# Performance work log

Hardware: AMD Instinct MI355X
Metric: run time of the kernel (lower is better)

Reference implementation:

```python
import jax, jax.numpy as jnp
import numpy as np

INPUT, HIDDEN, LAYERS, OUT = 512, 512, 2, 512
B, T = 128, 1024


def _gru_cell(x, h, w_ih, w_hh, b_ih, b_hh):
    # x: [B, D_in], h: [B, H]; w_ih: [3H, D_in], w_hh: [3H, H]
    gi = x @ w_ih.T + b_ih
    gh = h @ w_hh.T + b_hh
    i_r, i_z, i_n = jnp.split(gi, 3, axis=-1)
    h_r, h_z, h_n = jnp.split(gh, 3, axis=-1)
    r = jax.nn.sigmoid(i_r + h_r)
    z = jax.nn.sigmoid(i_z + h_z)
    n = jnp.tanh(i_n + r * h_n)
    return (1.0 - z) * n + z * h


def setup_inputs() -> dict:
    key = jax.random.key(0)
    ks = jax.random.split(key, 11)
    s = 1.0 / np.sqrt(HIDDEN)
    u = lambda k, shp: jax.random.uniform(k, shp, jnp.float32, -s, s)
    return {
        "x": jax.random.normal(ks[0], (B, T, INPUT), jnp.float32),
        "w_ih0": u(ks[1], (3 * HIDDEN, INPUT)),
        "w_hh0": u(ks[2], (3 * HIDDEN, HIDDEN)),
        "b_ih0": u(ks[3], (3 * HIDDEN,)),
        "b_hh0": u(ks[4], (3 * HIDDEN,)),
        "w_ih1": u(ks[5], (3 * HIDDEN, HIDDEN)),
        "w_hh1": u(ks[6], (3 * HIDDEN, HIDDEN)),
        "b_ih1": u(ks[7], (3 * HIDDEN,)),
        "b_hh1": u(ks[8], (3 * HIDDEN,)),
        "fc_w": u(ks[9], (OUT, HIDDEN)),
        "fc_b": u(ks[10], (OUT,)),
    }


def reference(x, w_ih0, w_hh0, b_ih0, b_hh0, w_ih1, w_hh1, b_ih1, b_hh1, fc_w, fc_b):
    xs = jnp.swapaxes(x, 0, 1)  # [T, B, INPUT]
    h0 = jnp.zeros((x.shape[0], HIDDEN), x.dtype)
    h1 = jnp.zeros((x.shape[0], HIDDEN), x.dtype)

    def step(carry, x_t):
        h0, h1 = carry
        h0 = _gru_cell(x_t, h0, w_ih0, w_hh0, b_ih0, b_hh0)
        h1 = _gru_cell(h0, h1, w_ih1, w_hh1, b_ih1, b_hh1)
        return (h0, h1), None

    (h0, h1), _ = jax.lax.scan(step, (h0, h1), xs)
    # final hidden of top layer -> fc (matches outs[-1].squeeze(); B>1 so squeeze is no-op)
    return h1 @ fc_w.T + fc_b
```

## Files before the change

### kernel.cpp

```cpp
#include <hip/hip_runtime.h>


#define TS   1024
#define HID  512
#define NWG  256
#define WGT  256

typedef __attribute__((ext_vector_type(8))) short bf16x8;
typedef __attribute__((ext_vector_type(4))) unsigned short u16x4;
typedef __attribute__((ext_vector_type(4))) float f32x4;

#define WS_SEQ      0
#define WS_FIN      2048
#define WS_HBUF     8192
#define HBUF_ELEMS  65536
#define WS_H1F      (WS_HBUF + 8 * HBUF_ELEMS * 2)
#define WS_ZERO     (WS_HBUF + 8 * HBUF_ELEMS * 2)

__device__ __forceinline__ unsigned short f2bf(float f) {
    unsigned u = __float_as_uint(f);
    u += 0x7FFFu + ((u >> 16) & 1u);
    return (unsigned short)(u >> 16);
}
__device__ __forceinline__ float bf2f(unsigned short s) {
    return __uint_as_float(((unsigned)s) << 16);
}
__device__ __forceinline__ float sigm(float v) { return 1.0f / (1.0f + __expf(-v)); }
__device__ __forceinline__ float tanh_(float v) { return 1.0f - 2.0f / (1.0f + __expf(2.0f * v)); }

__device__ __forceinline__ void st_llc8(void* p, unsigned long long v) {
    asm volatile("global_store_dwordx2 %0, %1, off sc0 sc1" :: "v"(p), "v"(v) : "memory");
}
__device__ __forceinline__ void st_llc16(void* p, f32x4 v) {
    asm volatile("global_store_dwordx4 %0, %1, off sc0 sc1" :: "v"(p), "v"(v) : "memory");
}
__device__ __forceinline__ bf16x8 ld_coh16(const unsigned short* p) {
    const unsigned long long* q = (const unsigned long long*)p;
    union { unsigned long long u[2]; bf16x8 v; } r;
    r.u[0] = __hip_atomic_load(q,     __ATOMIC_RELAXED, __HIP_MEMORY_SCOPE_AGENT);
    r.u[1] = __hip_atomic_load(q + 1, __ATOMIC_RELAXED, __HIP_MEMORY_SCOPE_AGENT);
    return r.v;
}
__device__ __forceinline__ f32x4 ld_coh16f(const float* p) {
    const unsigned long long* q = (const unsigned long long*)p;
    union { unsigned long long u[2]; f32x4 v; } r;
    r.u[0] = __hip_atomic_load(q,     __ATOMIC_RELAXED, __HIP_MEMORY_SCOPE_AGENT);
    r.u[1] = __hip_atomic_load(q + 1, __ATOMIC_RELAXED, __HIP_MEMORY_SCOPE_AGENT);
    return r.v;
}

__global__ void __launch_bounds__(WGT, 1)
gru_persistent(const float* __restrict__ x,
               const float* __restrict__ wi0, const float* __restrict__ wh0,
               const float* __restrict__ bi0, const float* __restrict__ bh0,
               const float* __restrict__ wi1, const float* __restrict__ wh1,
               const float* __restrict__ bi1, const float* __restrict__ bh1,
               const float* __restrict__ fcw, const float* __restrict__ fcb,
               float* __restrict__ out, unsigned char* __restrict__ ws)
{
    __shared__ float ldsRed[3][64][52];

    const int tid   = threadIdx.x;
    const int lane  = tid & 63;
    const int kq    = tid >> 6;
    const int wgid  = blockIdx.x;
    const int layer = wgid >> 7;
    const int wid   = wgid & 127;
    const int mt    = wid & 3;
    const int nt    = wid >> 2;
    const int l15   = lane & 15;
    const int l4    = lane >> 4;
    const int tile0 = mt * 2;
    const int gidx  = layer * 32 + nt;

    unsigned* seqA = (unsigned*)(ws + WS_SEQ + (size_t)mt * 256);
    unsigned* fin  = (unsigned*)(ws + WS_FIN);
    unsigned short* hbm = (unsigned short*)(ws + WS_HBUF);
    float* h1f = (float*)(ws + WS_H1F);

    unsigned short* h0hi[2] = { hbm + 0 * HBUF_ELEMS, hbm + 1 * HBUF_ELEMS };
    unsigned short* h0lo[2] = { hbm + 2 * HBUF_ELEMS, hbm + 3 * HBUF_ELEMS };
    unsigned short* h1hi[2] = { hbm + 4 * HBUF_ELEMS, hbm + 5 * HBUF_ELEMS };
    unsigned short* h1lo[2] = { hbm + 6 * HBUF_ELEMS, hbm + 7 * HBUF_ELEMS };

    bf16x8 wiR[4][3], whR[4][3];
    {
        const float* Wi = layer ? wi1 : wi0;
        const float* Wh = layer ? wh1 : wh0;
        #pragma unroll
        for (int kk = 0; kk < 4; ++kk) {
            const int kc = (kq << 2) + kk;
            #pragma unroll
            for (int g = 0; g < 3; ++g) {
                const int jg = g * HID + nt * 16 + l15;
                const float* pi = Wi + (size_t)jg * HID + kc * 32 + (l4 << 3);
                const float* ph = Wh + (size_t)jg * HID + kc * 32 + (l4 << 3);
                #pragma unroll
                for (int e = 0; e < 8; ++e) {
                    wiR[kk][g][e] = (short)f2bf(pi[e]);
                    whR[kk][g][e] = (short)f2bf(ph[e]);
                }
            }
        }
    }

    float br[4] = {0,0,0,0}, bz[4] = {0,0,0,0}, bni[4] = {0,0,0,0}, bnh[4] = {0,0,0,0};
    if (kq == 0) {
        const float* Bi = layer ? bi1 : bi0;
        const float* Bh = layer ? bh1 : bh0;
        int c0 = nt * 16 + (l4 << 2);
        #pragma unroll
        for (int r = 0; r < 4; ++r) {
            int j = c0 + r;
            br[r]  = Bi[j] + Bh[j];
            bz[r]  = Bi[HID + j] + Bh[HID + j];
            bni[r] = Bi[2 * HID + j];
            bnh[r] = Bh[2 * HID + j];
        }
    }

    float hold[2][4] = {{0,0,0,0},{0,0,0,0}};
    f32x4 acc_i[2][3], acc_h[2][3];
    #pragma unroll
    for (int m2 = 0; m2 < 2; ++m2)
        #pragma unroll
        for (int g = 0; g < 3; ++g) {
            acc_i[m2][g] = (f32x4){0.f,0.f,0.f,0.f};
            acc_h[m2][g] = (f32x4){0.f,0.f,0.f,0.f};
        }

    auto splitPack = [](float a, float b, unsigned& hiw, unsigned& low) {
        unsigned ba = __float_as_uint(a), bb = __float_as_uint(b);
        unsigned ha = ba & 0xFFFF0000u,   hb = bb & 0xFFFF0000u;
        float la = a - __uint_as_float(ha);
        float lb = b - __uint_as_float(hb);
        hiw = (ba >> 16) | hb;
        low = (__float_as_uint(la) >> 16) | (__float_as_uint(lb) & 0xFFFF0000u);
    };

    auto l0_input_mfma = [&](int sn) {
        #pragma unroll
        for (int kk = 0; kk < 4; ++kk) {
            const int kc = (kq << 2) + kk;
            #pragma unroll
            for (int m2 = 0; m2 < 2; ++m2) {
                const int m = (tile0 + m2) * 16 + l15;
                const int k = kc * 32 + (l4 << 3);
                const float* xp = x + ((size_t)m * TS + sn) * HID + k;
                f32x4 xa = *(const f32x4*)xp;
                f32x4 xb = *(const f32x4*)(xp + 4);
                union { unsigned u[4]; bf16x8 v; } hi, lo;
                splitPack(xa[0], xa[1], hi.u[0], lo.u[0]);
                splitPack(xa[2], xa[3], hi.u[1], lo.u[1]);
                splitPack(xb[0], xb[1], hi.u[2], lo.u[2]);
                splitPack(xb[2], xb[3], hi.u[3], lo.u[3]);
                #pragma unroll
                for (int g = 0; g < 3; ++g) {
                    acc_i[m2][g] = __builtin_amdgcn_mfma_f32_16x16x32_bf16(wiR[kk][g], lo.v, acc_i[m2][g], 0, 0, 0);
                    acc_i[m2][g] = __builtin_amdgcn_mfma_f32_16x16x32_bf16(wiR[kk][g], hi.v, acc_i[m2][g], 0, 0, 0);
                }
            }
        }
    };

    __syncthreads();
    if (layer == 0) l0_input_mfma(0);

    for (int s = 0; s <= TS; ++s) {
        const int wp = s & 1, rp = wp ^ 1;
        const bool active = layer ? (s >= 1) : (s < TS);
        if (active) {
            #pragma unroll
            for (int m2 = 0; m2 < 2; ++m2)
                #pragma unroll
                for (int g = 0; g < 3; ++g) {
                    acc_h[m2][g] = (f32x4){0.f,0.f,0.f,0.f};
                    if (layer) acc_i[m2][g] = (f32x4){0.f,0.f,0.f,0.f};
                }

            const unsigned short* pIhi = h0hi[rp];
            const unsigned short* pIlo = h0lo[rp];
            const unsigned short* pHhi = layer ? h1hi[rp] : h0hi[rp];
            const unsigned short* pHlo = layer ? h1lo[rp] : h0lo[rp];

            #pragma unroll
            for (int kk = 0; kk < 4; ++kk) {
                const int kc = (kq << 2) + kk;
                #pragma unroll
                for (int m2 = 0; m2 < 2; ++m2) {
                    const int fo = ((((tile0 + m2) * 16 + kc) * 64) + lane) * 8;
                    bf16x8 vHhi = ld_coh16(pHhi + fo);
                    bf16x8 vHlo = ld_coh16(pHlo + fo);
                    if (layer) {
                        bf16x8 vIhi = ld_coh16(pIhi + fo);
                        bf16x8 vIlo = ld_coh16(pIlo + fo);
                        #pragma unroll
                        for (int g = 0; g < 3; ++g) {
                            acc_i[m2][g] = __builtin_amdgcn_mfma_f32_16x16x32_bf16(wiR[kk][g], vIlo, acc_i[m2][g], 0, 0, 0);
                            acc_i[m2][g] = __builtin_amdgcn_mfma_f32_16x16x32_bf16(wiR[kk][g], vIhi, acc_i[m2][g], 0, 0, 0);
                        }
                    }
                    #pragma unroll
                    for (int g = 0; g < 3; ++g) {
                        acc_h[m2][g] = __builtin_amdgcn_mfma_f32_16x16x32_bf16(whR[kk][g], vHlo, acc_h[m2][g], 0, 0, 0);
                        acc_h[m2][g] = __builtin_amdgcn_mfma_f32_16x16x32_bf16(whR[kk][g], vHhi, acc_h[m2][g], 0, 0, 0);
                    }
                }
            }

            if (kq != 0) {
                float* p = &ldsRed[kq - 1][lane][0];
                #pragma unroll
                for (int m2 = 0; m2 < 2; ++m2)
                    #pragma unroll
                    for (int g = 0; g < 3; ++g) {
                        *(f32x4*)(p + m2 * 24 + g * 4)      = acc_i[m2][g];
                        *(f32x4*)(p + m2 * 24 + 12 + g * 4) = acc_h[m2][g];
                    }
            }
            __syncthreads();
            if (kq == 0) {
                #pragma unroll
                for (int q = 0; q < 3; ++q) {
                    const float* p = &ldsRed[q][lane][0];
                    #pragma unroll
                    for (int m2 = 0; m2 < 2; ++m2)
                        #pragma unroll
                        for (int g = 0; g < 3; ++g) {
                            acc_i[m2][g] += *(const f32x4*)(p + m2 * 24 + g * 4);
                            acc_h[m2][g] += *(const f32x4*)(p + m2 * 24 + 12 + g * 4);
                        }
                }
                unsigned short* dsthi = layer ? h1hi[wp] : h0hi[wp];
                unsigned short* dstlo = layer ? h1lo[wp] : h0lo[wp];
                const int klocal0 = ((nt & 1) << 4) + (l4 << 2);
                const int lanep = l15 | ((klocal0 >> 3) << 4);
                const int chunk = nt >> 1;
                #pragma unroll
                for (int m2 = 0; m2 < 2; ++m2) {
                    u16x4 shi, slo; f32x4 hv;
                    #pragma unroll
                    for (int r = 0; r < 4; ++r) {
                        float vr = acc_i[m2][0][r] + acc_h[m2][0][r] + br[r];
                        float vz = acc_i[m2][1][r] + acc_h[m2][1][r] + bz[r];
                        float rg = sigm(vr);
                        float zg = sigm(vz);
                        float ng = tanh_(acc_i[m2][2][r] + bni[r] + rg * (acc_h[m2][2][r] + bnh[r]));
                        float h  = (1.0f - zg) * ng + zg * hold[m2][r];
                        hold[m2][r] = h;
                        hv[r] = h;
                        unsigned short hb = f2bf(h);
                        shi[r] = hb;
                        slo[r] = f2bf(h - bf2f(hb));
                    }
                    const int eo = ((((tile0 + m2) * 16 + chunk) * 64) + lanep) * 8 + (klocal0 & 7);
                    st_llc8(dsthi + eo, __builtin_bit_cast(unsigned long long, shi));
                    st_llc8(dstlo + eo, __builtin_bit_cast(unsigned long long, slo));
                    if (layer && s == TS) {
                        const int m = (tile0 + m2) * 16 + l15;
                        const int kg0 = nt * 16 + (l4 << 2);
                        st_llc16(h1f + (size_t)m * HID + kg0, hv);
                    }
                }
            }
        }

        if (tid == 0) {
            asm volatile("s_waitcnt vmcnt(0)" ::: "memory");
            __hip_atomic_store(&seqA[gidx], (unsigned)(s + 1),
                               __ATOMIC_RELAXED, __HIP_MEMORY_SCOPE_AGENT);
        }

        if (layer == 0 && s + 1 < TS) {
            #pragma unroll
            for (int m2 = 0; m2 < 2; ++m2)
                #pragma unroll
                for (int g = 0; g < 3; ++g)
                    acc_i[m2][g] = (f32x4){0.f,0.f,0.f,0.f};
            l0_input_mfma(s + 1);
        }

        if (kq == 0) {
            const unsigned long long* sp =
                (const unsigned long long*)(seqA + ((lane & 15) << 2));
            const unsigned tgt = (unsigned)(s + 1);
            for (;;) {
                unsigned long long a = __hip_atomic_load(sp,     __ATOMIC_RELAXED, __HIP_MEMORY_SCOPE_AGENT);
                unsigned long long b = __hip_atomic_load(sp + 1, __ATOMIC_RELAXED, __HIP_MEMORY_SCOPE_AGENT);
                bool ok = ((unsigned)a >= tgt) && ((unsigned)(a >> 32) >= tgt) &&
                          ((unsigned)b >= tgt) && ((unsigned)(b >> 32) >= tgt);
                if (__all(ok)) break;
                __builtin_amdgcn_s_sleep(1);
            }
        }
        __syncthreads();
    }

    if (tid == 0) {
        asm volatile("s_waitcnt vmcnt(0)" ::: "memory");
        __hip_atomic_fetch_add(fin, 1u, __ATOMIC_RELAXED, __HIP_MEMORY_SCOPE_AGENT);
    }
    if (wgid < 64) {
        float* fw = (float*)ldsRed;
        const float* src = fcw + (size_t)wgid * 8 * HID;
        for (int i = tid; i < (8 * HID) / 4; i += WGT) {
            f32x4 v = *(const f32x4*)(src + i * 4);
            int row = (i * 4) >> 9;
            int kk  = (i * 4) & 511;
            *(f32x4*)(fw + row * 516 + kk) = v;
        }
        if (tid == 0) {
            while (__hip_atomic_load(fin, __ATOMIC_RELAXED, __HIP_MEMORY_SCOPE_AGENT) < (unsigned)NWG)
                __builtin_amdgcn_s_sleep(1);
        }
        __syncthreads();
        const int col = wgid * 8 + (tid & 7);
        const int m0  = tid >> 3;
        float a0 = fcb[col], a1 = a0, a2 = a0, a3 = a0;
        const float* fwr = fw + (tid & 7) * 516;
        for (int k = 0; k < HID; k += 4) {
            f32x4 wv  = *(const f32x4*)(fwr + k);
            f32x4 h0v = ld_coh16f(h1f + (size_t)(m0)      * HID + k);
            f32x4 h1v = ld_coh16f(h1f + (size_t)(m0 + 32) * HID + k);
            f32x4 h2v = ld_coh16f(h1f + (size_t)(m0 + 64) * HID + k);
            f32x4 h3v = ld_coh16f(h1f + (size_t)(m0 + 96) * HID + k);
            a0 += h0v[0]*wv[0] + h0v[1]*wv[1] + h0v[2]*wv[2] + h0v[3]*wv[3];
            a1 += h1v[0]*wv[0] + h1v[1]*wv[1] + h1v[2]*wv[2] + h1v[3]*wv[3];
            a2 += h2v[0]*wv[0] + h2v[1]*wv[1] + h2v[2]*wv[2] + h2v[3]*wv[3];
            a3 += h3v[0]*wv[0] + h3v[1]*wv[1] + h3v[2]*wv[2] + h3v[3]*wv[3];
        }
        out[(size_t)(m0)      * HID + col] = a0;
        out[(size_t)(m0 + 32) * HID + col] = a1;
        out[(size_t)(m0 + 64) * HID + col] = a2;
        out[(size_t)(m0 + 96) * HID + col] = a3;
    }
}

extern "C" void kernel_launch(void* const* d_in, const int* in_sizes, int n_in,
                              void* d_out, int out_size, void* d_ws, size_t ws_size,
                              hipStream_t stream) {
    (void)in_sizes; (void)n_in; (void)out_size; (void)ws_size;
    hipMemsetAsync(d_ws, 0, WS_ZERO, stream);
    gru_persistent<<<dim3(NWG), dim3(WGT), 0, stream>>>(
        (const float*)d_in[0],
        (const float*)d_in[1], (const float*)d_in[2],
        (const float*)d_in[3], (const float*)d_in[4],
        (const float*)d_in[5], (const float*)d_in[6],
        (const float*)d_in[7], (const float*)d_in[8],
        (const float*)d_in[9], (const float*)d_in[10],
        (float*)d_out, (unsigned char*)d_ws);
}
```

Before: 8.967 ms.

## Retile GRU work-groups to one M-tile by two N-tiles with batched coherent loads

Each work-group now owns one 16-row batch tile and 32 hidden columns per layer instead of two batch tiles by 16 columns. That doubles the register-resident weight fragments, halves the h-state loads per step, and shrinks each sync group to 16 producers per M-tile. The h-state and next-step x loads are now issued together as wide dwordx4 inline-asm loads followed by a single vmcnt wait, so their latency overlaps, replacing the serialized atomic 8-byte loads. The cost is higher VGPR pressure from the 6-fragment weight arrays, plus a flag poll that now reads only 8 lanes.

```diff
diff --git a/kernel.cpp b/kernel.cpp
--- a/kernel.cpp
+++ b/kernel.cpp
@@ -10,7 +10,6 @@
 typedef __attribute__((ext_vector_type(4))) unsigned short u16x4;
 typedef __attribute__((ext_vector_type(4))) float f32x4;
 
-#define WS_SEQ      0
 #define WS_FIN      2048
 #define WS_HBUF     8192
 #define HBUF_ELEMS  65536
@@ -34,12 +33,15 @@
 __device__ __forceinline__ void st_llc16(void* p, f32x4 v) {
     asm volatile("global_store_dwordx4 %0, %1, off sc0 sc1" :: "v"(p), "v"(v) : "memory");
 }
-__device__ __forceinline__ bf16x8 ld_coh16(const unsigned short* p) {
-    const unsigned long long* q = (const unsigned long long*)p;
-    union { unsigned long long u[2]; bf16x8 v; } r;
-    r.u[0] = __hip_atomic_load(q,     __ATOMIC_RELAXED, __HIP_MEMORY_SCOPE_AGENT);
-    r.u[1] = __hip_atomic_load(q + 1, __ATOMIC_RELAXED, __HIP_MEMORY_SCOPE_AGENT);
-    return r.v;
+__device__ __forceinline__ void ld_coh16_issue(bf16x8& d, const unsigned short* p) {
+    asm volatile("global_load_dwordx4 %0, %1, off sc0 sc1" : "=v"(d) : "v"(p));
+}
+__device__ __forceinline__ void ld16_issue(f32x4& d, const float* p) {
+    asm volatile("global_load_dwordx4 %0, %1, off" : "=v"(d) : "v"(p));
+}
+__device__ __forceinline__ void wait_vm0() {
+    asm volatile("s_waitcnt vmcnt(0)" ::: "memory");
+    __builtin_amdgcn_sched_barrier(0);
 }
 __device__ __forceinline__ f32x4 ld_coh16f(const float* p) {
     const unsigned long long* q = (const unsigned long long*)p;
@@ -58,7 +60,7 @@
                const float* __restrict__ fcw, const float* __restrict__ fcb,
                float* __restrict__ out, unsigned char* __restrict__ ws)
 {
-    __shared__ float ldsRed[3][64][52];
+    __shared__ float ldsRed[3][64][49];
 
     const int tid   = threadIdx.x;
     const int lane  = tid & 63;
@@ -66,14 +68,13 @@
     const int wgid  = blockIdx.x;
     const int layer = wgid >> 7;
     const int wid   = wgid & 127;
-    const int mt    = wid & 3;
-    const int nt    = wid >> 2;
+    const int mtile = wid & 7;
+    const int ntile = wid >> 3;
     const int l15   = lane & 15;
     const int l4    = lane >> 4;
-    const int tile0 = mt * 2;
-    const int gidx  = layer * 32 + nt;
-
-    unsigned* seqA = (unsigned*)(ws + WS_SEQ + (size_t)mt * 256);
+    const int gidx  = layer * 16 + ntile;
+
+    unsigned* seqA = (unsigned*)(ws + (size_t)mtile * 256);
     unsigned* fin  = (unsigned*)(ws + WS_FIN);
     unsigned short* hbm = (unsigned short*)(ws + WS_HBUF);
     float* h1f = (float*)(ws + WS_H1F);
@@ -83,7 +84,7 @@
     unsigned short* h1hi[2] = { hbm + 4 * HBUF_ELEMS, hbm + 5 * HBUF_ELEMS };
     unsigned short* h1lo[2] = { hbm + 6 * HBUF_ELEMS, hbm + 7 * HBUF_ELEMS };
 
-    bf16x8 wiR[4][3], whR[4][3];
+    bf16x8 wiR[4][6], whR[4][6];
     {
         const float* Wi = layer ? wi1 : wi0;
         const float* Wh = layer ? wh1 : wh0;
@@ -91,43 +92,51 @@
         for (int kk = 0; kk < 4; ++kk) {
             const int kc = (kq << 2) + kk;
             #pragma unroll
-            for (int g = 0; g < 3; ++g) {
-                const int jg = g * HID + nt * 16 + l15;
+            for (int f = 0; f < 6; ++f) {
+                const int g = f >> 1, n2 = f & 1;
+                const int jg = g * HID + ntile * 32 + n2 * 16 + l15;
                 const float* pi = Wi + (size_t)jg * HID + kc * 32 + (l4 << 3);
                 const float* ph = Wh + (size_t)jg * HID + kc * 32 + (l4 << 3);
                 #pragma unroll
                 for (int e = 0; e < 8; ++e) {
-                    wiR[kk][g][e] = (short)f2bf(pi[e]);
-                    whR[kk][g][e] = (short)f2bf(ph[e]);
-                }
-            }
-        }
-    }
-
-    float br[4] = {0,0,0,0}, bz[4] = {0,0,0,0}, bni[4] = {0,0,0,0}, bnh[4] = {0,0,0,0};
+                    wiR[kk][f][e] = (short)f2bf(pi[e]);
+                    whR[kk][f][e] = (short)f2bf(ph[e]);
+                }
+            }
+        }
+    }
+
+    float br[2][4], bz[2][4], bni[2][4], bnh[2][4];
     if (kq == 0) {
         const float* Bi = layer ? bi1 : bi0;
         const float* Bh = layer ? bh1 : bh0;
-        int c0 = nt * 16 + (l4 << 2);
-        #pragma unroll
-        for (int r = 0; r < 4; ++r) {
-            int j = c0 + r;
-            br[r]  = Bi[j] + Bh[j];
-            bz[r]  = Bi[HID + j] + Bh[HID + j];
-            bni[r] = Bi[2 * HID + j];
-            bnh[r] = Bh[2 * HID + j];
-        }
+        #pragma unroll
+        for (int n2 = 0; n2 < 2; ++n2)
+            #pragma unroll
+            for (int r = 0; r < 4; ++r) {
+                int j = ntile * 32 + n2 * 16 + (l4 << 2) + r;
+                br[n2][r]  = Bi[j] + Bh[j];
+                bz[n2][r]  = Bi[HID + j] + Bh[HID + j];
+                bni[n2][r] = Bi[2 * HID + j];
+                bnh[n2][r] = Bh[2 * HID + j];
+            }
+    } else {
+        #pragma unroll
+        for (int n2 = 0; n2 < 2; ++n2)
+            #pragma unroll
+            for (int r = 0; r < 4; ++r)
+                br[n2][r] = bz[n2][r] = bni[n2][r] = bnh[n2][r] = 0.f;
     }
 
     float hold[2][4] = {{0,0,0,0},{0,0,0,0}};
-    f32x4 acc_i[2][3], acc_h[2][3];
+    f32x4 acc_i[6], acc_h[6];
     #pragma unroll
-    for (int m2 = 0; m2 < 2; ++m2)
-        #pragma unroll
-        for (int g = 0; g < 3; ++g) {
-            acc_i[m2][g] = (f32x4){0.f,0.f,0.f,0.f};
-            acc_h[m2][g] = (f32x4){0.f,0.f,0.f,0.f};
-        }
+    for (int f = 0; f < 6; ++f) {
+        acc_i[f] = (f32x4){0.f,0.f,0.f,0.f};
+        acc_h[f] = (f32x4){0.f,0.f,0.f,0.f};
+    }
+
+    f32x4 xs[4][2];
 
     auto splitPack = [](float a, float b, unsigned& hiw, unsigned& low) {
         unsigned ba = __float_as_uint(a), bb = __float_as_uint(b);
@@ -138,85 +147,99 @@
         low = (__float_as_uint(la) >> 16) | (__float_as_uint(lb) & 0xFFFF0000u);
     };
 
-    auto l0_input_mfma = [&](int sn) {
+    auto do_window = [&]() {
+        #pragma unroll
+        for (int f = 0; f < 6; ++f) acc_i[f] = (f32x4){0.f,0.f,0.f,0.f};
         #pragma unroll
         for (int kk = 0; kk < 4; ++kk) {
-            const int kc = (kq << 2) + kk;
-            #pragma unroll
-            for (int m2 = 0; m2 < 2; ++m2) {
-                const int m = (tile0 + m2) * 16 + l15;
-                const int k = kc * 32 + (l4 << 3);
-                const float* xp = x + ((size_t)m * TS + sn) * HID + k;
-                f32x4 xa = *(const f32x4*)xp;
-                f32x4 xb = *(const f32x4*)(xp + 4);
-                union { unsigned u[4]; bf16x8 v; } hi, lo;
-                splitPack(xa[0], xa[1], hi.u[0], lo.u[0]);
-                splitPack(xa[2], xa[3], hi.u[1], lo.u[1]);
-                splitPack(xb[0], xb[1], hi.u[2], lo.u[2]);
-                splitPack(xb[2], xb[3], hi.u[3], lo.u[3]);
-                #pragma unroll
-                for (int g = 0; g < 3; ++g) {
-                    acc_i[m2][g] = __builtin_amdgcn_mfma_f32_16x16x32_bf16(wiR[kk][g], lo.v, acc_i[m2][g], 0, 0, 0);
-                    acc_i[m2][g] = __builtin_amdgcn_mfma_f32_16x16x32_bf16(wiR[kk][g], hi.v, acc_i[m2][g], 0, 0, 0);
-                }
+            union { unsigned u[4]; bf16x8 v; } hi, lo;
+            splitPack(xs[kk][0][0], xs[kk][0][1], hi.u[0], lo.u[0]);
+            splitPack(xs[kk][0][2], xs[kk][0][3], hi.u[1], lo.u[1]);
+            splitPack(xs[kk][1][0], xs[kk][1][1], hi.u[2], lo.u[2]);
+            splitPack(xs[kk][1][2], xs[kk][1][3], hi.u[3], lo.u[3]);
+            #pragma unroll
+            for (int f = 0; f < 6; ++f) {
+                acc_i[f] = __builtin_amdgcn_mfma_f32_16x16x32_bf16(wiR[kk][f], lo.v, acc_i[f], 0, 0, 0);
+                acc_i[f] = __builtin_amdgcn_mfma_f32_16x16x32_bf16(wiR[kk][f], hi.v, acc_i[f], 0, 0, 0);
             }
         }
     };
 
-    __syncthreads();
-    if (layer == 0) l0_input_mfma(0);
+    if (layer == 0) {
+        #pragma unroll
+        for (int kk = 0; kk < 4; ++kk) {
+            const int m = mtile * 16 + l15;
+            const int k = ((kq << 2) + kk) * 32 + (l4 << 3);
+            const float* xp = x + ((size_t)m * TS + 0) * HID + k;
+            ld16_issue(xs[kk][0], xp);
+            ld16_issue(xs[kk][1], xp + 4);
+        }
+        wait_vm0();
+        do_window();
+    }
 
     for (int s = 0; s <= TS; ++s) {
         const int wp = s & 1, rp = wp ^ 1;
         const bool active = layer ? (s >= 1) : (s < TS);
+        const bool window = (layer == 0) && (s + 1 < TS);
         if (active) {
             #pragma unroll
-            for (int m2 = 0; m2 < 2; ++m2)
-                #pragma unroll
-                for (int g = 0; g < 3; ++g) {
-                    acc_h[m2][g] = (f32x4){0.f,0.f,0.f,0.f};
-                    if (layer) acc_i[m2][g] = (f32x4){0.f,0.f,0.f,0.f};
-                }
+            for (int f = 0; f < 6; ++f) {
+                acc_h[f] = (f32x4){0.f,0.f,0.f,0.f};
+                if (layer) acc_i[f] = (f32x4){0.f,0.f,0.f,0.f};
+            }
 
             const unsigned short* pIhi = h0hi[rp];
             const unsigned short* pIlo = h0lo[rp];
             const unsigned short* pHhi = layer ? h1hi[rp] : h0hi[rp];
             const unsigned short* pHlo = layer ? h1lo[rp] : h0lo[rp];
 
+            bf16x8 hH[4][2], hI[4][2];
             #pragma unroll
             for (int kk = 0; kk < 4; ++kk) {
-                const int kc = (kq << 2) + kk;
-                #pragma unroll
-                for (int m2 = 0; m2 < 2; ++m2) {
-                    const int fo = ((((tile0 + m2) * 16 + kc) * 64) + lane) * 8;
-                    bf16x8 vHhi = ld_coh16(pHhi + fo);
-                    bf16x8 vHlo = ld_coh16(pHlo + fo);
-                    if (layer) {
-                        bf16x8 vIhi = ld_coh16(pIhi + fo);
-                        bf16x8 vIlo = ld_coh16(pIlo + fo);
-                        #pragma unroll
-                        for (int g = 0; g < 3; ++g) {
-                            acc_i[m2][g] = __builtin_amdgcn_mfma_f32_16x16x32_bf16(wiR[kk][g], vIlo, acc_i[m2][g], 0, 0, 0);
-                            acc_i[m2][g] = __builtin_amdgcn_mfma_f32_16x16x32_bf16(wiR[kk][g], vIhi, acc_i[m2][g], 0, 0, 0);
-                        }
+                const int fo = (((mtile * 16 + (kq << 2) + kk) * 64) + lane) * 8;
+                ld_coh16_issue(hH[kk][0], pHhi + fo);
+                ld_coh16_issue(hH[kk][1], pHlo + fo);
+                if (layer) {
+                    ld_coh16_issue(hI[kk][0], pIhi + fo);
+                    ld_coh16_issue(hI[kk][1], pIlo + fo);
+                }
+            }
+            if (window) {
+                #pragma unroll
+                for (int kk = 0; kk < 4; ++kk) {
+                    const int m = mtile * 16 + l15;
+                    const int k = ((kq << 2) + kk) * 32 + (l4 << 3);
+                    const float* xp = x + ((size_t)m * TS + (s + 1)) * HID + k;
+                    ld16_issue(xs[kk][0], xp);
+                    ld16_issue(xs[kk][1], xp + 4);
+                }
+            }
+            wait_vm0();
+
+            #pragma unroll
+            for (int kk = 0; kk < 4; ++kk) {
+                if (layer) {
+                    #pragma unroll
+                    for (int f = 0; f < 6; ++f) {
+                        acc_i[f] = __builtin_amdgcn_mfma_f32_16x16x32_bf16(wiR[kk][f], hI[kk][1], acc_i[f], 0, 0, 0);
+                        acc_i[f] = __builtin_amdgcn_mfma_f32_16x16x32_bf16(wiR[kk][f], hI[kk][0], acc_i[f], 0, 0, 0);
                     }
-                    #pragma unroll
-                    for (int g = 0; g < 3; ++g) {
-                        acc_h[m2][g] = __builtin_amdgcn_mfma_f32_16x16x32_bf16(whR[kk][g], vHlo, acc_h[m2][g], 0, 0, 0);
-                        acc_h[m2][g] = __builtin_amdgcn_mfma_f32_16x16x32_bf16(whR[kk][g], vHhi, acc_h[m2][g], 0, 0, 0);
-                    }
+                }
+                #pragma unroll
+                for (int f = 0; f < 6; ++f) {
+                    acc_h[f] = __builtin_amdgcn_mfma_f32_16x16x32_bf16(whR[kk][f], hH[kk][1], acc_h[f], 0, 0, 0);
+                    acc_h[f] = __builtin_amdgcn_mfma_f32_16x16x32_bf16(whR[kk][f], hH[kk][0], acc_h[f], 0, 0, 0);
                 }
             }
 
             if (kq != 0) {
                 float* p = &ldsRed[kq - 1][lane][0];
                 #pragma unroll
-                for (int m2 = 0; m2 < 2; ++m2)
-                    #pragma unroll
-                    for (int g = 0; g < 3; ++g) {
-                        *(f32x4*)(p + m2 * 24 + g * 4)      = acc_i[m2][g];
-                        *(f32x4*)(p + m2 * 24 + 12 + g * 4) = acc_h[m2][g];
-                    }
+                for (int f = 0; f < 6; ++f) {
+                    *(f32x4*)(p + f * 4)      = acc_i[f];
+                    *(f32x4*)(p + 24 + f * 4) = acc_h[f];
+                }
             }
             __syncthreads();
             if (kq == 0) {
@@ -224,42 +247,37 @@
                 for (int q = 0; q < 3; ++q) {
                     const float* p = &ldsRed[q][lane][0];
                     #pragma unroll
-                    for (int m2 = 0; m2 < 2; ++m2)
-                        #pragma unroll
-                        for (int g = 0; g < 3; ++g) {
-                            acc_i[m2][g] += *(const f32x4*)(p + m2 * 24 + g * 4);
-                            acc_h[m2][g] += *(const f32x4*)(p + m2 * 24 + 12 + g * 4);
-                        }
+                    for (int f = 0; f < 6; ++f) {
+                        acc_i[f] += *(const f32x4*)(p + f * 4);
+                        acc_h[f] += *(const f32x4*)(p + 24 + f * 4);
+                    }
                 }
                 unsigned short* dsthi = layer ? h1hi[wp] : h0hi[wp];
                 unsigned short* dstlo = layer ? h1lo[wp] : h0lo[wp];
-                const int klocal0 = ((nt & 1) << 4) + (l4 << 2);
-                const int lanep = l15 | ((klocal0 >> 3) << 4);
-                const int chunk = nt >> 1;
-                #pragma unroll
-                for (int m2 = 0; m2 < 2; ++m2) {
+                #pragma unroll
+                for (int n2 = 0; n2 < 2; ++n2) {
                     u16x4 shi, slo; f32x4 hv;
                     #pragma unroll
                     for (int r = 0; r < 4; ++r) {
-                        float vr = acc_i[m2][0][r] + acc_h[m2][0][r] + br[r];
-                        float vz = acc_i[m2][1][r] + acc_h[m2][1][r] + bz[r];
+                        float vr = acc_i[n2][r]     + acc_h[n2][r]     + br[n2][r];
+                        float vz = acc_i[2 + n2][r] + acc_h[2 + n2][r] + bz[n2][r];
                         float rg = sigm(vr);
                         float zg = sigm(vz);
-                        float ng = tanh_(acc_i[m2][2][r] + bni[r] + rg * (acc_h[m2][2][r] + bnh[r]));
-                        float h  = (1.0f - zg) * ng + zg * hold[m2][r];
-                        hold[m2][r] = h;
+                        float ng = tanh_(acc_i[4 + n2][r] + bni[n2][r] + rg * (acc_h[4 + n2][r] + bnh[n2][r]));
+                        float h  = (1.0f - zg) * ng + zg * hold[n2][r];
+                        hold[n2][r] = h;
                         hv[r] = h;
                         unsigned short hb = f2bf(h);
                         shi[r] = hb;
                         slo[r] = f2bf(h - bf2f(hb));
                     }
-                    const int eo = ((((tile0 + m2) * 16 + chunk) * 64) + lanep) * 8 + (klocal0 & 7);
+                    const int eo = (((mtile * 16 + ntile) * 64) + l15 + (n2 * 2 + (l4 >> 1)) * 16) * 8
+                                 + (l4 & 1) * 4;
                     st_llc8(dsthi + eo, __builtin_bit_cast(unsigned long long, shi));
                     st_llc8(dstlo + eo, __builtin_bit_cast(unsigned long long, slo));
                     if (layer && s == TS) {
-                        const int m = (tile0 + m2) * 16 + l15;
-                        const int kg0 = nt * 16 + (l4 << 2);
-                        st_llc16(h1f + (size_t)m * HID + kg0, hv);
+                        const int m = mtile * 16 + l15;
+                        st_llc16(h1f + (size_t)m * HID + ntile * 32 + n2 * 16 + (l4 << 2), hv);
                     }
                 }
             }
@@ -271,24 +289,20 @@
                                __ATOMIC_RELAXED, __HIP_MEMORY_SCOPE_AGENT);
         }
 
-        if (layer == 0 && s + 1 < TS) {
-            #pragma unroll
-            for (int m2 = 0; m2 < 2; ++m2)
-                #pragma unroll
-                for (int g = 0; g < 3; ++g)
-                    acc_i[m2][g] = (f32x4){0.f,0.f,0.f,0.f};
-            l0_input_mfma(s + 1);
-        }
+        if (window) do_window();
 
         if (kq == 0) {
+            const unsigned tgt = (unsigned)(s + 1);
             const unsigned long long* sp =
-                (const unsigned long long*)(seqA + ((lane & 15) << 2));
-            const unsigned tgt = (unsigned)(s + 1);
+                (const unsigned long long*)(seqA + ((lane & 7) << 2));
             for (;;) {
-                unsigned long long a = __hip_atomic_load(sp,     __ATOMIC_RELAXED, __HIP_MEMORY_SCOPE_AGENT);
-                unsigned long long b = __hip_atomic_load(sp + 1, __ATOMIC_RELAXED, __HIP_MEMORY_SCOPE_AGENT);
-                bool ok = ((unsigned)a >= tgt) && ((unsigned)(a >> 32) >= tgt) &&
-                          ((unsigned)b >= tgt) && ((unsigned)(b >> 32) >= tgt);
+                bool ok = true;
+                if (lane < 8) {
+                    unsigned long long a = __hip_atomic_load(sp,     __ATOMIC_RELAXED, __HIP_MEMORY_SCOPE_AGENT);
+                    unsigned long long b = __hip_atomic_load(sp + 1, __ATOMIC_RELAXED, __HIP_MEMORY_SCOPE_AGENT);
+                    ok = ((unsigned)a >= tgt) && ((unsigned)(a >> 32) >= tgt) &&
+                         ((unsigned)b >= tgt) && ((unsigned)(b >> 32) >= tgt);
+                }
                 if (__all(ok)) break;
                 __builtin_amdgcn_s_sleep(1);
             }
```

Result: faster. 8.781 ms (-2.1%).
